# Performance work log

Hardware: AMD Instinct MI355X
Metric: run time of the kernel (lower is better)

## Reference

```python
import jax, jax.numpy as jnp
import numpy as np

EPS = 1e-8
LN_EPS = 1e-5
NEG = -1e9
H, E, D, P = 4, 32, 8, 64          # heads, embed_dim, head_dim, particles (= input_dim)
N_LAYERS, N_CLS = 4, 2
N_BATCH = 2048
F_EXTRA = 60                        # x feature channels; F_EXTRA + 4 == P == input_dim


def _ln(x):
    m = jnp.mean(x, -1, keepdims=True)
    v = jnp.mean((x - m) ** 2, -1, keepdims=True)
    return (x - m) * jax.lax.rsqrt(v + LN_EPS)


def _lin(x, w, b):
    return x @ w.T + b


def _gelu(x):
    return jax.nn.gelu(x, approximate=False)


def _mha(q_in, kv, in_w, in_b, out_w, out_b, attn_bias, kpm):
    # torch nn.MultiheadAttention, batch_first=False. q_in: (L,N,E), kv: (S,N,E)
    L, N, _ = q_in.shape
    S = kv.shape[0]
    q = _lin(q_in, in_w[:E], in_b[:E]) * (D ** -0.5)
    k = _lin(kv, in_w[E:2 * E], in_b[E:2 * E])
    v = _lin(kv, in_w[2 * E:], in_b[2 * E:])
    q = q.reshape(L, N, H, D); k = k.reshape(S, N, H, D); v = v.reshape(S, N, H, D)
    s = jnp.einsum('lnhd,snhd->nhls', q, k)
    if attn_bias is not None:
        s = s + attn_bias.reshape(N, H, L, S)
    s = jnp.where(kpm[:, None, None, :], NEG, s)
    a = jax.nn.softmax(s, -1)
    o = jnp.einsum('nhls,snhd->lnhd', a, v).reshape(L, N, E)
    return _lin(o, out_w, out_b)


def _jet_features(v):
    # vectorized calculate_jet_features_; v: (N,4,P). All pair features are symmetric,
    # diagonal stays zero (python loop skipped i==j), features are detached.
    e, px, py, pz = v[:, 0], v[:, 1], v[:, 2], v[:, 3]
    pt = jnp.sqrt(px ** 2 + py ** 2 + EPS)
    y = 0.5 * jnp.log((e + pz + EPS) / (e - pz + EPS))
    phi = jnp.mod(jnp.arctan2(py, px + EPS), 2.0 * np.pi)   # already in [0, 2pi)
    r = lambda a: a[:, :, None]
    c = lambda a: a[:, None, :]
    dist = (r(px) + c(px)) ** 2 + (r(py) + c(py)) ** 2 + (r(pz) + c(pz)) ** 2
    delta = jnp.sqrt(jnp.abs((r(y) - c(y)) ** 2 + (r(phi) - c(phi)) ** 2))
    pmin = jnp.minimum(r(pt), c(pt))
    kt = pmin * delta
    z = pmin / (r(pt) + c(pt) + EPS)
    m2 = r(e) ** 2 + c(e) ** 2 - dist
    f = jnp.stack([delta, kt, z, m2], axis=1)               # (N,4,P,P)
    f = f * (1.0 - jnp.eye(v.shape[2], dtype=f.dtype))
    return jax.lax.stop_gradient(f)


def _conv2d(x, w, b, stride, pad):
    y = jax.lax.conv_general_dilated(x, w, (stride, stride), [(pad, pad), (pad, pad)],
                                     dimension_numbers=('NCHW', 'OIHW', 'NCHW'))
    return y + b[None, :, None, None]


def _forward(x, four_momenta, jet_inputs, bn_w, bn_b, e1_w, e1_b, e2_w, e2_b,
             c1_w, c1_b, c2_w, c2_b,
             pb_in_w, pb_in_b, pb_out_w, pb_out_b, pb_f1_w, pb_f1_b, pb_f2_w, pb_f2_b, pb_wres,
             cb_in_w, cb_in_b, cb_out_w, cb_out_b, cb_f1_w, cb_f1_b, cb_f2_w, cb_f2_b, cb_wres,
             cb_cattn, cls_token, norm_w, norm_b, m1_w, m1_b, mh_w, mh_b, mf_w, mf_b):
    N = x.shape[0]
    xc = jnp.concatenate([x, four_momenta], axis=1)                 # (N, P, P): channels == particles
    kpm = ~(jnp.arange(P)[None, :] < jet_inputs[:, 1][:, None])     # (N, P) True = padded key
    xb = jnp.transpose(xc, (0, 2, 1))                               # (N, C=P, L=input_dim)
    mu = jnp.mean(xb, axis=(0, 2), keepdims=True)
    var = jnp.var(xb, axis=(0, 2), keepdims=True)
    xb = (xb - mu) * jax.lax.rsqrt(var + LN_EPS) * bn_w[None, :, None] + bn_b[None, :, None]
    h = jnp.transpose(xb, (2, 0, 1))                                # (seq, N, P)
    h = _gelu(_lin(_ln(h), e1_w, e1_b))
    h = _gelu(_lin(_ln(h), e2_w, e2_b))                             # (P, N, E)
    # --- PairEmbed: pairwise kinematic features -> 2 convs -> per-head attention bias
    f = _jet_features(four_momenta)                                 # (N, 4, P, P)
    cpe = _conv2d(f, c1_w, c1_b, 4, 0)                              # (N, H, 16, 16)
    cpe = _conv2d(cpe, c2_w, c2_b, 2, 1)                            # (N, H, 9, 9)
    bias = cpe.reshape(N * H, 9, 9)
    bias = jnp.pad(bias, ((0, 0), (0, P - 9), (0, P - 9)))          # additive bias zero-padded to (N*H,P,P)
    # --- particle blocks
    for i in range(N_LAYERS):
        res = h
        a = _ln(h)
        a = _mha(a, a, pb_in_w[i], pb_in_b[i], pb_out_w[i], pb_out_b[i], bias, kpm)
        h = _ln(a) + res
        res = h
        g = _gelu(_lin(_ln(h), pb_f1_w[i], pb_f1_b[i]))
        g = _lin(_ln(g), pb_f2_w[i], pb_f2_b[i])
        h = g + pb_wres[i] * res
    # --- class-attention blocks
    kpm_cls = jnp.concatenate([jnp.zeros((N, 1), dtype=bool), kpm], axis=1)
    cls = jnp.broadcast_to(cls_token, (1, N, E))
    for i in range(N_CLS):
        res = cls
        u = _ln(jnp.concatenate([cls, h], axis=0))                  # pre_attn_norm on keys/values only
        a = _mha(cls, u, cb_in_w[i], cb_in_b[i], cb_out_w[i], cb_out_b[i], None, kpm_cls)
        # tbhd,h->tbdh then reshape flattens as (d, h) order, matching torch
        a = jnp.einsum('tbhd,h->tbdh', a.reshape(1, N, H, D), cb_cattn[i]).reshape(1, N, E)
        cls = _ln(a) + res
        res = cls
        g = _gelu(_lin(_ln(cls), cb_f1_w[i], cb_f1_b[i]))
        g = _lin(_ln(g), cb_f2_w[i], cb_f2_b[i])
        cls = g + cb_wres[i] * res
    # --- head: affine LayerNorm + MLP (the two transposes in MLP cancel)
    z = (_ln(cls) * norm_w + norm_b)[0]                             # (N, E)
    z = jax.nn.relu(_lin(z, m1_w, m1_b))
    z = jax.nn.relu(_lin(z, mh_w, mh_b))
    z = jax.nn.sigmoid(_lin(z, mf_w, mf_b))                         # (N, 1)
    return z.reshape(-1)


def setup_inputs():
    key = jax.random.key(0)
    ks = jax.random.split(key, 40)
    w = lambda k, s: (0.05 * jax.random.normal(k, s)).astype(jnp.float32)
    p3 = jax.random.normal(ks[0], (N_BATCH, 3, P), dtype=jnp.float32)
    en = jnp.sqrt(jnp.sum(p3 ** 2, axis=1, keepdims=True) + 0.1)    # physical: E > |pz|
    four_momenta = jnp.concatenate([en, p3], axis=1)
    return {
        'x': jax.random.normal(ks[1], (N_BATCH, F_EXTRA, P), dtype=jnp.float32),
        'four_momenta': four_momenta,
        'jet_inputs': jax.random.randint(ks[2], (N_BATCH, 2), 1, P + 1),
        'bn_w': jnp.ones((P,), jnp.float32), 'bn_b': jnp.zeros((P,), jnp.float32),
        'e1_w': w(ks[3], (64, P)), 'e1_b': w(ks[4], (64,)),
        'e2_w': w(ks[5], (E, 64)), 'e2_b': w(ks[6], (E,)),
        'c1_w': w(ks[7], (H, 4, 4, 4)), 'c1_b': w(ks[8], (H,)),
        'c2_w': w(ks[9], (H, H, 2, 2)), 'c2_b': w(ks[10], (H,)),
        'pb_in_w': w(ks[11], (N_LAYERS, 3 * E, E)), 'pb_in_b': w(ks[12], (N_LAYERS, 3 * E)),
        'pb_out_w': w(ks[13], (N_LAYERS, E, E)), 'pb_out_b': w(ks[14], (N_LAYERS, E)),
        'pb_f1_w': w(ks[15], (N_LAYERS, 2 * E, E)), 'pb_f1_b': w(ks[16], (N_LAYERS, 2 * E)),
        'pb_f2_w': w(ks[17], (N_LAYERS, E, 2 * E)), 'pb_f2_b': w(ks[18], (N_LAYERS, E)),
        'pb_wres': jnp.ones((N_LAYERS, E), jnp.float32),
        'cb_in_w': w(ks[19], (N_CLS, 3 * E, E)), 'cb_in_b': w(ks[20], (N_CLS, 3 * E)),
        'cb_out_w': w(ks[21], (N_CLS, E, E)), 'cb_out_b': w(ks[22], (N_CLS, E)),
        'cb_f1_w': w(ks[23], (N_CLS, 2 * E, E)), 'cb_f1_b': w(ks[24], (N_CLS, 2 * E)),
        'cb_f2_w': w(ks[25], (N_CLS, E, 2 * E)), 'cb_f2_b': w(ks[26], (N_CLS, E)),
        'cb_wres': jnp.ones((N_CLS, E), jnp.float32),
        'cb_cattn': jnp.ones((N_CLS, H), jnp.float32),
        'cls_token': w(ks[27], (1, 1, E)),
        'norm_w': jnp.ones((E,), jnp.float32), 'norm_b': jnp.zeros((E,), jnp.float32),
        'm1_w': w(ks[28], (32, E)), 'm1_b': w(ks[29], (32,)),
        'mh_w': w(ks[30], (32, 32)), 'mh_b': w(ks[31], (32,)),
        'mf_w': w(ks[32], (1, 32)), 'mf_b': w(ks[33], (1,)),
    }


def reference(x, four_momenta, jet_inputs, bn_w, bn_b, e1_w, e1_b, e2_w, e2_b,
              c1_w, c1_b, c2_w, c2_b,
              pb_in_w, pb_in_b, pb_out_w, pb_out_b, pb_f1_w, pb_f1_b, pb_f2_w, pb_f2_b, pb_wres,
              cb_in_w, cb_in_b, cb_out_w, cb_out_b, cb_f1_w, cb_f1_b, cb_f2_w, cb_f2_b, cb_wres,
              cb_cattn, cls_token, norm_w, norm_b, m1_w, m1_b, mh_w, mh_b, mf_w, mf_b):
    return _forward(x, four_momenta, jet_inputs, bn_w, bn_b, e1_w, e1_b, e2_w, e2_b,
                    c1_w, c1_b, c2_w, c2_b,
                    pb_in_w, pb_in_b, pb_out_w, pb_out_b, pb_f1_w, pb_f1_b, pb_f2_w, pb_f2_b, pb_wres,
                    cb_in_w, cb_in_b, cb_out_w, cb_out_b, cb_f1_w, cb_f1_b, cb_f2_w, cb_f2_b, cb_wres,
                    cb_cattn, cls_token, norm_w, norm_b, m1_w, m1_b, mh_w, mh_b, mf_w, mf_b)
```

## Files before the change

kernel.cpp:

```cpp
#include <hip/hip_runtime.h>


__device__ __forceinline__ float4 ld4(const float* p){ return *reinterpret_cast<const float4*>(p); }
__device__ __forceinline__ void st4(float* p, float4 v){ *reinterpret_cast<float4*>(p) = v; }
__device__ __forceinline__ float dot4(float4 a, float4 b){ return a.x*b.x + a.y*b.y + a.z*b.z + a.w*b.w; }
__device__ __forceinline__ float geluf(float v){ return 0.5f*v*(1.0f + erff(v*0.70710678118654752f)); }

__global__ void bn_stats_partial(const float* __restrict__ x, const float* __restrict__ fm,
                                 float* __restrict__ part) {
  int p  = threadIdx.x & 63;
  int rg = threadIdx.x >> 6;
  float s = 0.f, s2 = 0.f;
  for (int R = blockIdx.x*4 + rg; R < 2048*64; R += 1024) {
    int n_ = R >> 6, c = R & 63;
    float v = (c < 60) ? x[n_*3840 + c*64 + p] : fm[n_*256 + (c-60)*64 + p];
    s += v; s2 += v*v;
  }
  __shared__ float sm[256], sm2[256];
  sm[threadIdx.x] = s; sm2[threadIdx.x] = s2;
  __syncthreads();
  if (threadIdx.x < 64) {
    part[blockIdx.x*128 + p]      = sm[p]+sm[64+p]+sm[128+p]+sm[192+p];
    part[blockIdx.x*128 + 64 + p] = sm2[p]+sm2[64+p]+sm2[128+p]+sm2[192+p];
  }
}

__global__ void bn_stats_final(const float* __restrict__ part, float* __restrict__ stats) {
  int p = threadIdx.x;
  float s = 0.f, s2 = 0.f;
  for (int b = 0; b < 256; b++){ s += part[b*128+p]; s2 += part[b*128+64+p]; }
  float mean = s * (1.f/131072.f);
  float var  = s2 * (1.f/131072.f) - mean*mean;
  stats[p]      = mean;
  stats[64+p]   = rsqrtf(var + 1e-5f);
}

__device__ __forceinline__ void ln_rows32(const float* src, float* dst, int tid){
  int r = tid>>2, g = tid&3;
  const float* row = src + r*36 + g*8;
  float4 a = ld4(row), b = ld4(row+4);
  float s = a.x+a.y+a.z+a.w + b.x+b.y+b.z+b.w;
  s += __shfl_xor(s,1); s += __shfl_xor(s,2);
  float mean = s * 0.03125f;
  float4 da = make_float4(a.x-mean,a.y-mean,a.z-mean,a.w-mean);
  float4 db = make_float4(b.x-mean,b.y-mean,b.z-mean,b.w-mean);
  float q = dot4(da,da) + dot4(db,db);
  q += __shfl_xor(q,1); q += __shfl_xor(q,2);
  float irs = rsqrtf(q*0.03125f + 1e-5f);
  float* drow = dst + r*36 + g*8;
  st4(drow,   make_float4(da.x*irs, da.y*irs, da.z*irs, da.w*irs));
  st4(drow+4, make_float4(db.x*irs, db.y*irs, db.z*irs, db.w*irs));
}

__device__ __forceinline__ void ln_rows64(const float* src, float* dst, int tid){
  int r = tid>>2, g = tid&3;
  const float* row = src + r*68 + g*16;
  float4 v0 = ld4(row), v1 = ld4(row+4), v2 = ld4(row+8), v3 = ld4(row+12);
  float s = v0.x+v0.y+v0.z+v0.w + v1.x+v1.y+v1.z+v1.w
          + v2.x+v2.y+v2.z+v2.w + v3.x+v3.y+v3.z+v3.w;
  s += __shfl_xor(s,1); s += __shfl_xor(s,2);
  float mean = s * 0.015625f;
  float4 d0 = make_float4(v0.x-mean,v0.y-mean,v0.z-mean,v0.w-mean);
  float4 d1 = make_float4(v1.x-mean,v1.y-mean,v1.z-mean,v1.w-mean);
  float4 d2 = make_float4(v2.x-mean,v2.y-mean,v2.z-mean,v2.w-mean);
  float4 d3 = make_float4(v3.x-mean,v3.y-mean,v3.z-mean,v3.w-mean);
  float q = dot4(d0,d0)+dot4(d1,d1)+dot4(d2,d2)+dot4(d3,d3);
  q += __shfl_xor(q,1); q += __shfl_xor(q,2);
  float irs = rsqrtf(q*0.015625f + 1e-5f);
  float* drow = dst + r*68 + g*16;
  st4(drow,    make_float4(d0.x*irs,d0.y*irs,d0.z*irs,d0.w*irs));
  st4(drow+4,  make_float4(d1.x*irs,d1.y*irs,d1.z*irs,d1.w*irs));
  st4(drow+8,  make_float4(d2.x*irs,d2.y*irs,d2.z*irs,d2.w*irs));
  st4(drow+12, make_float4(d3.x*irs,d3.y*irs,d3.z*irs,d3.w*irs));
}

__global__ __launch_bounds__(256, 3) void k_embed(
    const float* __restrict__ x, const float* __restrict__ fm,
    const float* __restrict__ stats,
    const float* __restrict__ bn_w, const float* __restrict__ bn_b,
    const float* __restrict__ e1w, const float* __restrict__ e1b,
    const float* __restrict__ e2w, const float* __restrict__ e2b,
    const float* __restrict__ c1w_g, const float* __restrict__ c1b_g,
    const float* __restrict__ c2w_g, const float* __restrict__ c2b_g,
    float* __restrict__ G_h, float* __restrict__ G_bias)
{
  const int n   = blockIdx.x;
  const int tid = threadIdx.x;

  __shared__ __align__(16) float SX[64*68];
  __shared__ __align__(16) float SY[64*68];
  __shared__ __align__(16) float SW[4448];
  __shared__ float SSTAT[128];

  float* PQ  = SY;
  float* C1O = SY + 448;
  float* CW  = SY + 1472;

  if (tid < 64) {
    float mu = stats[tid], rs = stats[64+tid];
    float sc = rs * bn_w[tid];
    SSTAT[tid]      = sc;
    SSTAT[64+tid]   = bn_b[tid] - mu*sc;
  }
  if (tid < 64) {
    int p = tid;
    float e_  = fm[n*256 + p];
    float px_ = fm[n*256 + 64 + p];
    float py_ = fm[n*256 + 128 + p];
    float pz_ = fm[n*256 + 192 + p];
    float pt_ = sqrtf(px_*px_ + py_*py_ + 1e-8f);
    float y_  = 0.5f * logf((e_ + pz_ + 1e-8f) / (e_ - pz_ + 1e-8f));
    float ph_ = atan2f(py_, px_ + 1e-8f);
    if (ph_ < 0.f) ph_ += 6.283185307179586f;
    PQ[0*64+p]=e_; PQ[1*64+p]=px_; PQ[2*64+p]=py_; PQ[3*64+p]=pz_;
    PQ[4*64+p]=pt_; PQ[5*64+p]=y_; PQ[6*64+p]=ph_;
  }
  CW[tid] = c1w_g[tid];
  if (tid < 4)  CW[256+tid] = c1b_g[tid];
  if (tid < 64) CW[260+tid] = c2w_g[tid];
  if (tid < 4)  CW[324+tid] = c2b_g[tid];
  __syncthreads();

  {
    int ho = tid>>4, wo = tid&15;
    float a0=0.f,a1=0.f,a2=0.f,a3=0.f;
    #pragma unroll 1
    for (int kh=0; kh<4; kh++){
      int r = ho*4+kh;
      float er=PQ[r], pxr=PQ[64+r], pyr=PQ[128+r], pzr=PQ[192+r], ptr_=PQ[256+r], yr=PQ[320+r], phr=PQ[384+r];
      #pragma unroll
      for (int kw=0; kw<4; kw++){
        int c = wo*4+kw;
        if (r == c) continue;
        float ec=PQ[c], pxc=PQ[64+c], pyc=PQ[128+c], pzc=PQ[192+c], ptc=PQ[256+c], yc=PQ[320+c], phc=PQ[384+c];
        float dy = yr-yc, dp = phr-phc;
        float delta = sqrtf(fabsf(dy*dy + dp*dp));
        float pmin = fminf(ptr_, ptc);
        float kt = pmin * delta;
        float zz = pmin / (ptr_ + ptc + 1e-8f);
        float sx_ = pxr+pxc, sy_ = pyr+pyc, sz_ = pzr+pzc;
        float m2 = er*er + ec*ec - (sx_*sx_ + sy_*sy_ + sz_*sz_);
        int wb = kh*4+kw;
        a0 += delta*CW[0*64+wb] + kt*CW[0*64+16+wb] + zz*CW[0*64+32+wb] + m2*CW[0*64+48+wb];
        a1 += delta*CW[1*64+wb] + kt*CW[1*64+16+wb] + zz*CW[1*64+32+wb] + m2*CW[1*64+48+wb];
        a2 += delta*CW[2*64+wb] + kt*CW[2*64+16+wb] + zz*CW[2*64+32+wb] + m2*CW[2*64+48+wb];
        a3 += delta*CW[3*64+wb] + kt*CW[3*64+16+wb] + zz*CW[3*64+32+wb] + m2*CW[3*64+48+wb];
      }
    }
    C1O[0*256 + tid] = a0 + CW[256+0];
    C1O[1*256 + tid] = a1 + CW[256+1];
    C1O[2*256 + tid] = a2 + CW[256+2];
    C1O[3*256 + tid] = a3 + CW[256+3];
  }
  __syncthreads();

  for (int idx = tid; idx < 324; idx += 256) {
    int co = idx/81, rem = idx%81, i = rem/9, j = rem%9;
    float s = CW[324+co];
    #pragma unroll
    for (int ci=0; ci<4; ci++){
      #pragma unroll
      for (int kh=0; kh<2; kh++){
        int ri = 2*i - 1 + kh;
        if (ri < 0 || ri >= 16) continue;
        #pragma unroll
        for (int kw=0; kw<2; kw++){
          int cj = 2*j - 1 + kw;
          if (cj < 0 || cj >= 16) continue;
          s += CW[260 + co*16 + ci*4 + kh*2 + kw] * C1O[ci*256 + ri*16 + cj];
        }
      }
    }
    G_bias[n*324 + idx] = s;
  }
  {
    int p4 = (tid & 15) * 4;
    float sc0 = SSTAT[p4], sc1 = SSTAT[p4+1], sc2 = SSTAT[p4+2], sc3 = SSTAT[p4+3];
    float sh0 = SSTAT[64+p4], sh1 = SSTAT[64+p4+1], sh2 = SSTAT[64+p4+2], sh3 = SSTAT[64+p4+3];
    for (int c = tid>>4; c < 64; c += 16) {
      float4 v = (c < 60) ? ld4(x + n*3840 + c*64 + p4) : ld4(fm + n*256 + (c-60)*64 + p4);
      st4(&SX[c*68 + p4], make_float4(v.x*sc0+sh0, v.y*sc1+sh1, v.z*sc2+sh2, v.w*sc3+sh3));
    }
  }
  __syncthreads();

  ln_rows64(SX, SY, tid);
  for (int idx = tid; idx < 1024; idx += 256) st4(&SW[(idx>>4)*68 + (idx&15)*4], ld4(e1w + idx*4));
  if (tid < 64) SW[4352+tid] = e1b[tid];
  __syncthreads();

  {
    int tg = tid>>4, og = tid&15;
    float acc[4][4];
    #pragma unroll
    for (int o=0;o<4;o++){ float b = SW[4352+o*16+og];
      #pragma unroll
      for (int i=0;i<4;i++) acc[i][o] = b; }
    #pragma unroll 2
    for (int j=0;j<64;j+=4){
      float4 av[4], wv[4];
      #pragma unroll
      for (int i=0;i<4;i++) av[i] = ld4(SY + (tg*4+i)*68 + j);
      #pragma unroll
      for (int o=0;o<4;o++) wv[o] = ld4(SW + (o*16+og)*68 + j);
      #pragma unroll
      for (int i=0;i<4;i++)
        #pragma unroll
        for (int o=0;o<4;o++) acc[i][o] += dot4(av[i], wv[o]);
    }
    __syncthreads();
    #pragma unroll
    for (int i=0;i<4;i++)
      #pragma unroll
      for (int o=0;o<4;o++) SX[(tg*4+i)*68 + o*16+og] = geluf(acc[i][o]);
  }
  __syncthreads();

  ln_rows64(SX, SY, tid);
  for (int idx = tid; idx < 512; idx += 256) st4(&SW[(idx>>4)*68 + (idx&15)*4], ld4(e2w + idx*4));
  if (tid < 32) SW[4352+tid] = e2b[tid];
  __syncthreads();

  {
    int tg = tid>>4, og = tid&15;
    float acc[4][2];
    #pragma unroll
    for (int o=0;o<2;o++){ float b = SW[4352+o*16+og];
      #pragma unroll
      for (int i=0;i<4;i++) acc[i][o] = b; }
    #pragma unroll 2
    for (int j=0;j<64;j+=4){
      float4 av[4], wv[2];
      #pragma unroll
      for (int i=0;i<4;i++) av[i] = ld4(SY + (tg*4+i)*68 + j);
      #pragma unroll
      for (int o=0;o<2;o++) wv[o] = ld4(SW + (o*16+og)*68 + j);
      #pragma unroll
      for (int i=0;i<4;i++)
        #pragma unroll
        for (int o=0;o<2;o++) acc[i][o] += dot4(av[i], wv[o]);
    }
    #pragma unroll
    for (int i=0;i<4;i++)
      #pragma unroll
      for (int o=0;o<2;o++) G_h[n*2048 + (tg*4+i)*32 + o*16+og] = geluf(acc[i][o]);
  }
}

__global__ __launch_bounds__(256, 3) void k_layer(
    const int* __restrict__ ji,
    const float* __restrict__ in_w,  const float* __restrict__ in_b,
    const float* __restrict__ out_w, const float* __restrict__ out_b,
    const float* __restrict__ f1w,   const float* __restrict__ f1b,
    const float* __restrict__ f2w,   const float* __restrict__ f2b,
    const float* __restrict__ wres,
    float* __restrict__ G_h, const float* __restrict__ G_bias)
{
  const int n   = blockIdx.x;
  const int tid = threadIdx.x;

  __shared__ __align__(16) float SH[64*36];
  __shared__ __align__(16) float SX[64*36];
  __shared__ __align__(16) float SY[64*68];
  __shared__ __align__(16) float SW[3584];
  __shared__ int s_njet;

  if (tid == 0) s_njet = ji[n*2+1];
  float b9[9];
  {
    int hh = tid>>6, l = tid&63;
    if (l < 9) {
      #pragma unroll
      for (int j=0;j<9;j++) b9[j] = G_bias[n*324 + hh*81 + l*9 + j];
    } else {
      #pragma unroll
      for (int j=0;j<9;j++) b9[j] = 0.f;
    }
  }
  for (int idx = tid; idx < 512; idx += 256) {
    float4 v = ld4(G_h + n*2048 + idx*4);
    int t = idx>>3, e = (idx&7)*4;
    st4(&SH[t*36 + e], v);
  }
  __syncthreads();

  ln_rows32(SH, SX, tid);
  for (int idx = tid; idx < 768; idx += 256) st4(&SW[(idx>>3)*36 + (idx&7)*4], ld4(in_w + idx*4));
  if (tid < 96) SW[3456+tid] = in_b[tid];
  __syncthreads();

  {
    int tg = tid>>4, og = tid&15;
    float acc[4][4];
    #pragma unroll
    for (int o=0;o<4;o++){ float b = SW[3456+32+o*16+og];
      #pragma unroll
      for (int i=0;i<4;i++) acc[i][o] = b; }
    #pragma unroll 2
    for (int j=0;j<32;j+=4){
      float4 av[4], wv[4];
      #pragma unroll
      for (int i=0;i<4;i++) av[i] = ld4(SX + (tg*4+i)*36 + j);
      #pragma unroll
      for (int o=0;o<4;o++) wv[o] = ld4(SW + (32+o*16+og)*36 + j);
      #pragma unroll
      for (int i=0;i<4;i++)
        #pragma unroll
        for (int o=0;o<4;o++) acc[i][o] += dot4(av[i], wv[o]);
    }
    #pragma unroll
    for (int i=0;i<4;i++)
      #pragma unroll
      for (int o=0;o<4;o++){
        int ew = 32 + o*16+og, t = tg*4+i;
        if (ew < 64) SY[(ew-32)*68 + t] = acc[i][o];
        else         SY[2176 + (ew-64)*68 + t] = acc[i][o];
      }
  }
  __syncthreads();

  float od[8];
  {
    int hh = tid>>6, l = tid&63;
    float qd[8];
    #pragma unroll
    for (int d=0;d<8;d++){
      int e = hh*8+d;
      float a_ = SW[3456+e];
      #pragma unroll
      for (int k=0;k<8;k++) a_ += dot4(ld4(SX + l*36 + k*4), ld4(SW + e*36 + k*4));
      qd[d] = a_ * 0.35355339059327373f;
    }
    int njet = s_njet;
    float m = -3.4e38f, lsum = 0.f;
    #pragma unroll
    for (int d=0;d<8;d++) od[d] = 0.f;
    #pragma unroll 1
    for (int s0 = 0; s0 < 64; s0 += 16) {
      if (s0 >= njet) break;
      float sc[16];
      #pragma unroll
      for (int j=0;j<16;j++) sc[j]=0.f;
      #pragma unroll
      for (int d=0;d<8;d++){
        const float* kr = SY + (hh*8+d)*68 + s0;
        float qv = qd[d];
        #pragma unroll
        for (int j=0;j<16;j+=4){
          float4 kv4 = ld4(kr+j);
          sc[j]  +=qv*kv4.x; sc[j+1]+=qv*kv4.y;
          sc[j+2]+=qv*kv4.z; sc[j+3]+=qv*kv4.w;
        }
      }
      float cm = -3.4e38f;
      if (s0 != 0 && s0 + 16 <= njet) {
        #pragma unroll
        for (int j=0;j<16;j++) cm = fmaxf(cm, sc[j]);
      } else {
        #pragma unroll
        for (int j=0;j<16;j++){
          int s = s0+j;
          float a_ = sc[j];
          if (s0 == 0 && l < 9 && j < 9) a_ += b9[j];
          a_ = (s >= njet) ? -1000000000.0f : a_;
          sc[j] = a_;
          cm = fmaxf(cm, a_);
        }
      }
      float nm = fmaxf(m, cm);
      float corr = __expf(m - nm);
      lsum *= corr;
      #pragma unroll
      for (int d=0;d<8;d++) od[d] *= corr;
      #pragma unroll
      for (int j=0;j<16;j++){ sc[j] = __expf(sc[j]-nm); lsum += sc[j]; }
      #pragma unroll
      for (int d=0;d<8;d++){
        const float* vr = SY + 2176 + (hh*8+d)*68 + s0;
        float a_ = 0.f;
        #pragma unroll
        for (int j=0;j<16;j+=4){
          float4 vv = ld4(vr+j);
          a_ += sc[j]*vv.x + sc[j+1]*vv.y + sc[j+2]*vv.z + sc[j+3]*vv.w;
        }
        od[d] += a_;
      }
      m = nm;
    }
    float inv = 1.f/lsum;
    #pragma unroll
    for (int d=0;d<8;d++) od[d] *= inv;
  }
  __syncthreads();
  {
    int hh = tid>>6, l = tid&63;
    st4(&SX[l*36 + hh*8],     make_float4(od[0],od[1],od[2],od[3]));
    st4(&SX[l*36 + hh*8 + 4], make_float4(od[4],od[5],od[6],od[7]));
  }
  for (int idx = tid; idx < 256; idx += 256) st4(&SW[(idx>>3)*36 + (idx&7)*4], ld4(out_w + idx*4));
  if (tid < 32) SW[3456+tid] = out_b[tid];
  __syncthreads();

  {
    int tg = tid>>4, og = tid&15;
    float acc[4][2];
    #pragma unroll
    for (int o=0;o<2;o++){ float b = SW[3456+o*16+og];
      #pragma unroll
      for (int i=0;i<4;i++) acc[i][o] = b; }
    #pragma unroll 2
    for (int j=0;j<32;j+=4){
      float4 av[4], wv[2];
      #pragma unroll
      for (int i=0;i<4;i++) av[i] = ld4(SX + (tg*4+i)*36 + j);
      #pragma unroll
      for (int o=0;o<2;o++) wv[o] = ld4(SW + (o*16+og)*36 + j);
      #pragma unroll
      for (int i=0;i<4;i++)
        #pragma unroll
        for (int o=0;o<2;o++) acc[i][o] += dot4(av[i], wv[o]);
    }
    #pragma unroll
    for (int i=0;i<4;i++)
      #pragma unroll
      for (int o=0;o<2;o++) SY[(tg*4+i)*36 + o*16+og] = acc[i][o];
  }
  __syncthreads();

  {
    int r = tid>>2, g = tid&3;
    const float* row = SY + r*36 + g*8;
    float4 a = ld4(row), b = ld4(row+4);
    float s = a.x+a.y+a.z+a.w + b.x+b.y+b.z+b.w;
    s += __shfl_xor(s,1); s += __shfl_xor(s,2);
    float mean = s * 0.03125f;
    float4 da = make_float4(a.x-mean,a.y-mean,a.z-mean,a.w-mean);
    float4 db = make_float4(b.x-mean,b.y-mean,b.z-mean,b.w-mean);
    float q = dot4(da,da) + dot4(db,db);
    q += __shfl_xor(q,1); q += __shfl_xor(q,2);
    float irs = rsqrtf(q*0.03125f + 1e-5f);
    float* hrow = SH + r*36 + g*8;
    float4 ha = ld4(hrow), hb = ld4(hrow+4);
    st4(hrow,   make_float4(da.x*irs+ha.x, da.y*irs+ha.y, da.z*irs+ha.z, da.w*irs+ha.w));
    st4(hrow+4, make_float4(db.x*irs+hb.x, db.y*irs+hb.y, db.z*irs+hb.z, db.w*irs+hb.w));
  }
  __syncthreads();

  ln_rows32(SH, SX, tid);
  for (int idx = tid; idx < 512; idx += 256) st4(&SW[(idx>>3)*36 + (idx&7)*4], ld4(f1w + idx*4));
  if (tid < 64) SW[3456+tid] = f1b[tid];
  __syncthreads();

  {
    int tg = tid>>4, og = tid&15;
    float acc[4][4];
    #pragma unroll
    for (int o=0;o<4;o++){ float b = SW[3456+o*16+og];
      #pragma unroll
      for (int i=0;i<4;i++) acc[i][o] = b; }
    #pragma unroll 2
    for (int j=0;j<32;j+=4){
      float4 av[4], wv[4];
      #pragma unroll
      for (int i=0;i<4;i++) av[i] = ld4(SX + (tg*4+i)*36 + j);
      #pragma unroll
      for (int o=0;o<4;o++) wv[o] = ld4(SW + (o*16+og)*36 + j);
      #pragma unroll
      for (int i=0;i<4;i++)
        #pragma unroll
        for (int o=0;o<4;o++) acc[i][o] += dot4(av[i], wv[o]);
    }
    #pragma unroll
    for (int i=0;i<4;i++)
      #pragma unroll
      for (int o=0;o<4;o++) SY[(tg*4+i)*68 + o*16+og] = geluf(acc[i][o]);
  }
  __syncthreads();

  {
    int r = tid>>2, g = tid&3;
    float* row = SY + r*68 + g*16;
    float4 v0 = ld4(row), v1 = ld4(row+4), v2 = ld4(row+8), v3 = ld4(row+12);
    float s = v0.x+v0.y+v0.z+v0.w + v1.x+v1.y+v1.z+v1.w
            + v2.x+v2.y+v2.z+v2.w + v3.x+v3.y+v3.z+v3.w;
    s += __shfl_xor(s,1); s += __shfl_xor(s,2);
    float mean = s * 0.015625f;
    float4 d0 = make_float4(v0.x-mean,v0.y-mean,v0.z-mean,v0.w-mean);
    float4 d1 = make_float4(v1.x-mean,v1.y-mean,v1.z-mean,v1.w-mean);
    float4 d2 = make_float4(v2.x-mean,v2.y-mean,v2.z-mean,v2.w-mean);
    float4 d3 = make_float4(v3.x-mean,v3.y-mean,v3.z-mean,v3.w-mean);
    float q = dot4(d0,d0)+dot4(d1,d1)+dot4(d2,d2)+dot4(d3,d3);
    q += __shfl_xor(q,1); q += __shfl_xor(q,2);
    float irs = rsqrtf(q*0.015625f + 1e-5f);
    st4(row,    make_float4(d0.x*irs,d0.y*irs,d0.z*irs,d0.w*irs));
    st4(row+4,  make_float4(d1.x*irs,d1.y*irs,d1.z*irs,d1.w*irs));
    st4(row+8,  make_float4(d2.x*irs,d2.y*irs,d2.z*irs,d2.w*irs));
    st4(row+12, make_float4(d3.x*irs,d3.y*irs,d3.z*irs,d3.w*irs));
  }
  for (int idx = tid; idx < 512; idx += 256) st4(&SW[(idx>>4)*68 + (idx&15)*4], ld4(f2w + idx*4));
  if (tid < 32){ SW[3456+tid] = f2b[tid]; SW[3488+tid] = wres[tid]; }
  __syncthreads();

  {
    int tg = tid>>4, og = tid&15;
    float acc[4][2];
    #pragma unroll
    for (int o=0;o<2;o++){ float b = SW[3456+o*16+og];
      #pragma unroll
      for (int i=0;i<4;i++) acc[i][o] = b; }
    #pragma unroll 2
    for (int j=0;j<64;j+=4){
      float4 av[4], wv[2];
      #pragma unroll
      for (int i=0;i<4;i++) av[i] = ld4(SY + (tg*4+i)*68 + j);
      #pragma unroll
      for (int o=0;o<2;o++) wv[o] = ld4(SW + (o*16+og)*68 + j);
      #pragma unroll
      for (int i=0;i<4;i++)
        #pragma unroll
        for (int o=0;o<2;o++) acc[i][o] += dot4(av[i], wv[o]);
    }
    #pragma unroll
    for (int i=0;i<4;i++)
      #pragma unroll
      for (int o=0;o<2;o++){
        int e = o*16+og, t = tg*4+i;
        G_h[n*2048 + t*32 + e] = acc[i][o] + SW[3488+e]*SH[t*36+e];
      }
  }
}

__global__ __launch_bounds__(256, 3) void k_cls(
    const int* __restrict__ ji,
    const float* __restrict__ cb_in_w, const float* __restrict__ cb_in_b,
    const float* __restrict__ cb_out_w, const float* __restrict__ cb_out_b,
    const float* __restrict__ cb_f1_w, const float* __restrict__ cb_f1_b,
    const float* __restrict__ cb_f2_w, const float* __restrict__ cb_f2_b,
    const float* __restrict__ cb_wres, const float* __restrict__ cb_cattn,
    const float* __restrict__ cls_tok, const float* __restrict__ norm_w, const float* __restrict__ norm_b,
    const float* __restrict__ m1w, const float* __restrict__ m1b,
    const float* __restrict__ mhw, const float* __restrict__ mhb,
    const float* __restrict__ mfw, const float* __restrict__ mfb,
    const float* __restrict__ G_h, float* __restrict__ out)
{
  const int n   = blockIdx.x;
  const int tid = threadIdx.x;

  __shared__ __align__(16) float SX[64*36];
  __shared__ __align__(16) float SY[64*68];
  __shared__ __align__(16) float SW[3584];
  __shared__ __align__(16) float SV[320];
  __shared__ __align__(16) float csh[32];
  __shared__ int s_njet;

  if (tid == 0) s_njet = ji[n*2+1];
  for (int idx = tid; idx < 512; idx += 256) {
    float4 v = ld4(G_h + n*2048 + idx*4);
    int t = idx>>3, e = (idx&7)*4;
    st4(&SX[t*36 + e], v);
  }
  __syncthreads();

  ln_rows32(SX, SX, tid);
  if (tid < 32) csh[tid] = cls_tok[tid];
  __syncthreads();

  #pragma unroll 1
  for (int cl = 0; cl < 2; cl++) {
    const float* iw = cb_in_w + cl*3072;
    const float* ib = cb_in_b + cl*96;

    if (tid < 32) {
      float v = csh[tid];
      float s = v;
      s += __shfl_xor(s,1); s += __shfl_xor(s,2); s += __shfl_xor(s,4); s += __shfl_xor(s,8); s += __shfl_xor(s,16);
      float mean = s * 0.03125f;
      float d = v - mean;
      float q = d*d;
      q += __shfl_xor(q,1); q += __shfl_xor(q,2); q += __shfl_xor(q,4); q += __shfl_xor(q,8); q += __shfl_xor(q,16);
      float irs = rsqrtf(q*0.03125f + 1e-5f);
      SV[tid] = d*irs;
    }
    for (int idx = tid; idx < 768; idx += 256) st4(&SW[(idx>>3)*36 + (idx&7)*4], ld4(iw + idx*4));
    if (tid < 96) SW[3456+tid] = ib[tid];
    __syncthreads();

    if (tid < 32) {
      int e = tid;
      float a_ = SW[3456+e];
      #pragma unroll
      for (int k=0;k<8;k++) a_ += dot4(ld4(&csh[k*4]), ld4(SW + e*36 + k*4));
      SV[32+e] = a_ * 0.35355339059327373f;
    }
    if (tid < 64) {
      int ew = 32 + tid;
      float a_ = SW[3456+ew];
      #pragma unroll
      for (int k=0;k<8;k++) a_ += dot4(ld4(SV + k*4), ld4(SW + ew*36 + k*4));
      if (ew < 64) SY[(ew-32)*68] = a_;
      else         SY[2176 + (ew-64)*68] = a_;
    }
    {
      int tg = tid>>4, og = tid&15;
      float acc[4][4];
      #pragma unroll
      for (int o=0;o<4;o++){ float b = SW[3456+32+o*16+og];
        #pragma unroll
        for (int i=0;i<4;i++) acc[i][o] = b; }
      #pragma unroll 2
      for (int j=0;j<32;j+=4){
        float4 av[4], wv[4];
        #pragma unroll
        for (int i=0;i<4;i++) av[i] = ld4(SX + (tg*4+i)*36 + j);
        #pragma unroll
        for (int o=0;o<4;o++) wv[o] = ld4(SW + (32+o*16+og)*36 + j);
        #pragma unroll
        for (int i=0;i<4;i++)
          #pragma unroll
          for (int o=0;o<4;o++) acc[i][o] += dot4(av[i], wv[o]);
      }
      #pragma unroll
      for (int i=0;i<4;i++)
        #pragma unroll
        for (int o=0;o<4;o++){
          int ew = 32 + o*16+og, s = tg*4+i + 1;
          if (ew < 64) SY[(ew-32)*68 + s] = acc[i][o];
          else         SY[2176 + (ew-64)*68 + s] = acc[i][o];
        }
    }
    __syncthreads();

    {
      int hh = tid>>6, l = tid&63;
      int njet = s_njet;
      float q8[8];
      #pragma unroll
      for (int d=0;d<8;d++) q8[d] = SV[32 + hh*8 + d];
      float sc_ = 0.f;
      #pragma unroll
      for (int d=0;d<8;d++) sc_ += q8[d]*SY[(hh*8+d)*68 + l];
      if (l > 0 && (l-1) >= njet) sc_ = -1000000000.0f;
      float sc64 = 0.f;
      if (l == 0){
        #pragma unroll
        for (int d=0;d<8;d++) sc64 += q8[d]*SY[(hh*8+d)*68 + 64];
        if (63 >= njet) sc64 = -1000000000.0f;
      }
      float mx = sc_;
      if (l == 0) mx = fmaxf(mx, sc64);
      mx = fmaxf(mx, __shfl_xor(mx,1));  mx = fmaxf(mx, __shfl_xor(mx,2));
      mx = fmaxf(mx, __shfl_xor(mx,4));  mx = fmaxf(mx, __shfl_xor(mx,8));
      mx = fmaxf(mx, __shfl_xor(mx,16)); mx = fmaxf(mx, __shfl_xor(mx,32));
      float p   = __expf(sc_ - mx);
      float p64 = (l==0) ? __expf(sc64 - mx) : 0.f;
      float ssum = p + p64;
      ssum += __shfl_xor(ssum,1); ssum += __shfl_xor(ssum,2); ssum += __shfl_xor(ssum,4);
      ssum += __shfl_xor(ssum,8); ssum += __shfl_xor(ssum,16); ssum += __shfl_xor(ssum,32);
      float inv = 1.f/ssum;
      #pragma unroll
      for (int d=0;d<8;d++){
        float term = p * SY[2176 + (hh*8+d)*68 + l];
        if (l == 0) term += p64 * SY[2176 + (hh*8+d)*68 + 64];
        term += __shfl_xor(term,1); term += __shfl_xor(term,2); term += __shfl_xor(term,4);
        term += __shfl_xor(term,8); term += __shfl_xor(term,16); term += __shfl_xor(term,32);
        if (l == 0) SV[64 + hh*8 + d] = term*inv;
      }
    }
    __syncthreads();

    if (tid < 32) {
      int e = tid;
      const float* wrow = cb_out_w + (cl*32 + e)*32;
      float a_ = cb_out_b[cl*32 + e];
      #pragma unroll
      for (int j=0;j<32;j++) a_ += SV[64+j]*wrow[j];
      float ca = cb_cattn[cl*4 + (e>>3)];
      SV[96 + (e&7)*4 + (e>>3)] = a_*ca;
    }
    if (tid < 32) {
      float v = SV[96+tid];
      float s = v;
      s += __shfl_xor(s,1); s += __shfl_xor(s,2); s += __shfl_xor(s,4); s += __shfl_xor(s,8); s += __shfl_xor(s,16);
      float mean = s * 0.03125f;
      float d = v - mean;
      float q = d*d;
      q += __shfl_xor(q,1); q += __shfl_xor(q,2); q += __shfl_xor(q,4); q += __shfl_xor(q,8); q += __shfl_xor(q,16);
      float irs = rsqrtf(q*0.03125f + 1e-5f);
      csh[tid] = d*irs + csh[tid];
    }
    if (tid < 32) {
      float v = csh[tid];
      float s = v;
      s += __shfl_xor(s,1); s += __shfl_xor(s,2); s += __shfl_xor(s,4); s += __shfl_xor(s,8); s += __shfl_xor(s,16);
      float mean = s * 0.03125f;
      float d = v - mean;
      float q = d*d;
      q += __shfl_xor(q,1); q += __shfl_xor(q,2); q += __shfl_xor(q,4); q += __shfl_xor(q,8); q += __shfl_xor(q,16);
      float irs = rsqrtf(q*0.03125f + 1e-5f);
      SV[tid] = d*irs;
    }
    if (tid < 64) {
      int o = tid;
      const float* wrow = cb_f1_w + (cl*64+o)*32;
      float a_ = cb_f1_b[cl*64+o];
      #pragma unroll
      for (int j=0;j<32;j++) a_ += SV[j]*wrow[j];
      SV[128+o] = geluf(a_);
    }
    if (tid < 64) {
      float v = SV[128+tid];
      float s = v;
      s += __shfl_xor(s,1); s += __shfl_xor(s,2); s += __shfl_xor(s,4); s += __shfl_xor(s,8);
      s += __shfl_xor(s,16); s += __shfl_xor(s,32);
      float mean = s * 0.015625f;
      float d = v - mean;
      float q = d*d;
      q += __shfl_xor(q,1); q += __shfl_xor(q,2); q += __shfl_xor(q,4); q += __shfl_xor(q,8);
      q += __shfl_xor(q,16); q += __shfl_xor(q,32);
      float irs = rsqrtf(q*0.015625f + 1e-5f);
      SV[192+tid] = d*irs;
    }
    if (tid < 32) {
      int e = tid;
      const float* wrow = cb_f2_w + (cl*32+e)*64;
      float a_ = cb_f2_b[cl*32+e];
      #pragma unroll
      for (int j=0;j<64;j++) a_ += SV[192+j]*wrow[j];
      csh[e] = a_ + cb_wres[cl*32+e]*csh[e];
    }
  }

  if (tid < 32) {
    float v = csh[tid];
    float s = v;
    s += __shfl_xor(s,1); s += __shfl_xor(s,2); s += __shfl_xor(s,4); s += __shfl_xor(s,8); s += __shfl_xor(s,16);
    float mean = s * 0.03125f;
    float d = v - mean;
    float q = d*d;
    q += __shfl_xor(q,1); q += __shfl_xor(q,2); q += __shfl_xor(q,4); q += __shfl_xor(q,8); q += __shfl_xor(q,16);
    float irs = rsqrtf(q*0.03125f + 1e-5f);
    SV[tid] = d*irs*norm_w[tid] + norm_b[tid];
  }
  if (tid < 32) {
    float a_ = m1b[tid];
    const float* wrow = m1w + tid*32;
    #pragma unroll
    for (int j=0;j<32;j++) a_ += SV[j]*wrow[j];
    SV[64+tid] = fmaxf(a_, 0.f);
  }
  if (tid < 32) {
    float a_ = mhb[tid];
    const float* wrow = mhw + tid*32;
    #pragma unroll
    for (int j=0;j<32;j++) a_ += SV[64+j]*wrow[j];
    SV[128+tid] = fmaxf(a_, 0.f);
  }
  if (tid == 0) {
    float a_ = mfb[0];
    #pragma unroll
    for (int j=0;j<32;j++) a_ += SV[128+j]*mfw[j];
    out[n] = 1.f/(1.f + expf(-a_));
  }
}

extern "C" void kernel_launch(void* const* d_in, const int* in_sizes, int n_in,
                              void* d_out, int out_size, void* d_ws, size_t ws_size,
                              hipStream_t stream) {
  (void)in_sizes; (void)n_in; (void)out_size; (void)ws_size;
  const float* x     = (const float*)d_in[0];
  const float* fm    = (const float*)d_in[1];
  const int*   ji    = (const int*)  d_in[2];
  const float* bn_w  = (const float*)d_in[3];
  const float* bn_b  = (const float*)d_in[4];
  const float* e1w   = (const float*)d_in[5];
  const float* e1b   = (const float*)d_in[6];
  const float* e2w   = (const float*)d_in[7];
  const float* e2b   = (const float*)d_in[8];
  const float* c1w   = (const float*)d_in[9];
  const float* c1b   = (const float*)d_in[10];
  const float* c2w   = (const float*)d_in[11];
  const float* c2b   = (const float*)d_in[12];
  const float* pb_in_w  = (const float*)d_in[13];
  const float* pb_in_b  = (const float*)d_in[14];
  const float* pb_out_w = (const float*)d_in[15];
  const float* pb_out_b = (const float*)d_in[16];
  const float* pb_f1_w  = (const float*)d_in[17];
  const float* pb_f1_b  = (const float*)d_in[18];
  const float* pb_f2_w  = (const float*)d_in[19];
  const float* pb_f2_b  = (const float*)d_in[20];
  const float* pb_wres  = (const float*)d_in[21];
  const float* cb_in_w  = (const float*)d_in[22];
  const float* cb_in_b  = (const float*)d_in[23];
  const float* cb_out_w = (const float*)d_in[24];
  const float* cb_out_b = (const float*)d_in[25];
  const float* cb_f1_w  = (const float*)d_in[26];
  const float* cb_f1_b  = (const float*)d_in[27];
  const float* cb_f2_w  = (const float*)d_in[28];
  const float* cb_f2_b  = (const float*)d_in[29];
  const float* cb_wres  = (const float*)d_in[30];
  const float* cb_cattn = (const float*)d_in[31];
  const float* cls_tok  = (const float*)d_in[32];
  const float* norm_w   = (const float*)d_in[33];
  const float* norm_b   = (const float*)d_in[34];
  const float* m1w      = (const float*)d_in[35];
  const float* m1b      = (const float*)d_in[36];
  const float* mhw      = (const float*)d_in[37];
  const float* mhb      = (const float*)d_in[38];
  const float* mfw      = (const float*)d_in[39];
  const float* mfb      = (const float*)d_in[40];

  float* part   = (float*)d_ws;
  float* stats  = part + 32768;
  float* G_h    = part + 40960;
  float* G_bias = G_h + 2048*2048;

  bn_stats_partial<<<256, 256, 0, stream>>>(x, fm, part);
  bn_stats_final<<<1, 64, 0, stream>>>(part, stats);
  k_embed<<<2048, 256, 0, stream>>>(x, fm, stats, bn_w, bn_b, e1w, e1b, e2w, e2b,
                                    c1w, c1b, c2w, c2b, G_h, G_bias);
  for (int li = 0; li < 4; li++) {
    k_layer<<<2048, 256, 0, stream>>>(ji,
        pb_in_w + li*3072, pb_in_b + li*96,
        pb_out_w + li*1024, pb_out_b + li*32,
        pb_f1_w + li*2048, pb_f1_b + li*64,
        pb_f2_w + li*2048, pb_f2_b + li*32,
        pb_wres + li*32, G_h, G_bias);
  }
  k_cls<<<2048, 256, 0, stream>>>(ji, cb_in_w, cb_in_b, cb_out_w, cb_out_b,
                                  cb_f1_w, cb_f1_b, cb_f2_w, cb_f2_b,
                                  cb_wres, cb_cattn, cls_tok, norm_w, norm_b,
                                  m1w, m1b, mhw, mhb, mfw, mfb, G_h, (float*)d_out);
}
```

Baseline: 512.5 us.

## Skip per-token work for padded particles beyond each jet's count

Each kernel reads the per-jet particle count and gates the layernorm, projection, MLP and output stages on whether a wave's 16-token slice contains any real particles. It also loads only the hidden rows up to the rounded particle count and zero-fills keys for inactive slices in the class-attention kernel. Whole wavefronts of work on masked padding tokens are skipped. This relies on padded tokens never affecting outputs, and padded rows of the hidden state become stale or uninitialised.

```diff
diff --git a/kernel.cpp b/kernel.cpp
--- a/kernel.cpp
+++ b/kernel.cpp
@@ -76,6 +76,7 @@
 
 __global__ __launch_bounds__(256, 3) void k_embed(
     const float* __restrict__ x, const float* __restrict__ fm,
+    const int* __restrict__ ji,
     const float* __restrict__ stats,
     const float* __restrict__ bn_w, const float* __restrict__ bn_b,
     const float* __restrict__ e1w, const float* __restrict__ e1b,
@@ -86,6 +87,8 @@
 {
   const int n   = blockIdx.x;
   const int tid = threadIdx.x;
+  const int njet = ji[n*2+1];
+  const bool wact = ((tid>>6)<<4) < njet;
 
   __shared__ __align__(16) float SX[64*68];
   __shared__ __align__(16) float SY[64*68];
@@ -184,7 +187,7 @@
   }
   __syncthreads();
 
-  ln_rows64(SX, SY, tid);
+  if (wact) ln_rows64(SX, SY, tid);
   for (int idx = tid; idx < 1024; idx += 256) st4(&SW[(idx>>4)*68 + (idx&15)*4], ld4(e1w + idx*4));
   if (tid < 64) SW[4352+tid] = e1b[tid];
   __syncthreads();
@@ -196,32 +199,36 @@
     for (int o=0;o<4;o++){ float b = SW[4352+o*16+og];
       #pragma unroll
       for (int i=0;i<4;i++) acc[i][o] = b; }
-    #pragma unroll 2
-    for (int j=0;j<64;j+=4){
-      float4 av[4], wv[4];
-      #pragma unroll
-      for (int i=0;i<4;i++) av[i] = ld4(SY + (tg*4+i)*68 + j);
-      #pragma unroll
-      for (int o=0;o<4;o++) wv[o] = ld4(SW + (o*16+og)*68 + j);
+    if (wact) {
+      #pragma unroll 2
+      for (int j=0;j<64;j+=4){
+        float4 av[4], wv[4];
+        #pragma unroll
+        for (int i=0;i<4;i++) av[i] = ld4(SY + (tg*4+i)*68 + j);
+        #pragma unroll
+        for (int o=0;o<4;o++) wv[o] = ld4(SW + (o*16+og)*68 + j);
+        #pragma unroll
+        for (int i=0;i<4;i++)
+          #pragma unroll
+          for (int o=0;o<4;o++) acc[i][o] += dot4(av[i], wv[o]);
+      }
+    }
+    __syncthreads();
+    if (wact) {
       #pragma unroll
       for (int i=0;i<4;i++)
         #pragma unroll
-        for (int o=0;o<4;o++) acc[i][o] += dot4(av[i], wv[o]);
-    }
-    __syncthreads();
-    #pragma unroll
-    for (int i=0;i<4;i++)
-      #pragma unroll
-      for (int o=0;o<4;o++) SX[(tg*4+i)*68 + o*16+og] = geluf(acc[i][o]);
-  }
-  __syncthreads();
-
-  ln_rows64(SX, SY, tid);
+        for (int o=0;o<4;o++) SX[(tg*4+i)*68 + o*16+og] = geluf(acc[i][o]);
+    }
+  }
+  __syncthreads();
+
+  if (wact) ln_rows64(SX, SY, tid);
   for (int idx = tid; idx < 512; idx += 256) st4(&SW[(idx>>4)*68 + (idx&15)*4], ld4(e2w + idx*4));
   if (tid < 32) SW[4352+tid] = e2b[tid];
   __syncthreads();
 
-  {
+  if (wact) {
     int tg = tid>>4, og = tid&15;
     float acc[4][2];
     #pragma unroll
@@ -258,14 +265,15 @@
 {
   const int n   = blockIdx.x;
   const int tid = threadIdx.x;
+  const int njet = ji[n*2+1];
+  const int nt16 = (njet + 15) & ~15;
+  const bool wact = ((tid>>6)<<4) < njet;
 
   __shared__ __align__(16) float SH[64*36];
   __shared__ __align__(16) float SX[64*36];
   __shared__ __align__(16) float SY[64*68];
   __shared__ __align__(16) float SW[3584];
-  __shared__ int s_njet;
-
-  if (tid == 0) s_njet = ji[n*2+1];
+
   float b9[9];
   {
     int hh = tid>>6, l = tid&63;
@@ -277,19 +285,19 @@
       for (int j=0;j<9;j++) b9[j] = 0.f;
     }
   }
-  for (int idx = tid; idx < 512; idx += 256) {
+  for (int idx = tid; idx < (nt16<<3); idx += 256) {
     float4 v = ld4(G_h + n*2048 + idx*4);
     int t = idx>>3, e = (idx&7)*4;
     st4(&SH[t*36 + e], v);
   }
   __syncthreads();
 
-  ln_rows32(SH, SX, tid);
+  if (wact) ln_rows32(SH, SX, tid);
   for (int idx = tid; idx < 768; idx += 256) st4(&SW[(idx>>3)*36 + (idx&7)*4], ld4(in_w + idx*4));
   if (tid < 96) SW[3456+tid] = in_b[tid];
   __syncthreads();
 
-  {
+  if (wact) {
     int tg = tid>>4, og = tid&15;
     float acc[4][4];
     #pragma unroll
@@ -331,13 +339,11 @@
       for (int k=0;k<8;k++) a_ += dot4(ld4(SX + l*36 + k*4), ld4(SW + e*36 + k*4));
       qd[d] = a_ * 0.35355339059327373f;
     }
-    int njet = s_njet;
     float m = -3.4e38f, lsum = 0.f;
     #pragma unroll
     for (int d=0;d<8;d++) od[d] = 0.f;
     #pragma unroll 1
-    for (int s0 = 0; s0 < 64; s0 += 16) {
-      if (s0 >= njet) break;
+    for (int s0 = 0; s0 < njet; s0 += 16) {
       float sc[16];
       #pragma unroll
       for (int j=0;j<16;j++) sc[j]=0.f;
@@ -401,7 +407,7 @@
   if (tid < 32) SW[3456+tid] = out_b[tid];
   __syncthreads();
 
-  {
+  if (wact) {
     int tg = tid>>4, og = tid&15;
     float acc[4][2];
     #pragma unroll
@@ -427,7 +433,7 @@
   }
   __syncthreads();
 
-  {
+  if (wact) {
     int r = tid>>2, g = tid&3;
     const float* row = SY + r*36 + g*8;
     float4 a = ld4(row), b = ld4(row+4);
@@ -446,12 +452,12 @@
   }
   __syncthreads();
 
-  ln_rows32(SH, SX, tid);
+  if (wact) ln_rows32(SH, SX, tid);
   for (int idx = tid; idx < 512; idx += 256) st4(&SW[(idx>>3)*36 + (idx&7)*4], ld4(f1w + idx*4));
   if (tid < 64) SW[3456+tid] = f1b[tid];
   __syncthreads();
 
-  {
+  if (wact) {
     int tg = tid>>4, og = tid&15;
     float acc[4][4];
     #pragma unroll
@@ -477,7 +483,7 @@
   }
   __syncthreads();
 
-  {
+  if (wact) {
     int r = tid>>2, g = tid&3;
     float* row = SY + r*68 + g*16;
     float4 v0 = ld4(row), v1 = ld4(row+4), v2 = ld4(row+8), v3 = ld4(row+12);
@@ -501,7 +507,7 @@
   if (tid < 32){ SW[3456+tid] = f2b[tid]; SW[3488+tid] = wres[tid]; }
   __syncthreads();
 
-  {
+  if (wact) {
     int tg = tid>>4, og = tid&15;
     float acc[4][2];
     #pragma unroll
@@ -545,23 +551,24 @@
 {
   const int n   = blockIdx.x;
   const int tid = threadIdx.x;
+  const int njet = ji[n*2+1];
+  const int nt16 = (njet + 15) & ~15;
+  const bool wact = ((tid>>6)<<4) < njet;
 
   __shared__ __align__(16) float SX[64*36];
   __shared__ __align__(16) float SY[64*68];
   __shared__ __align__(16) float SW[3584];
   __shared__ __align__(16) float SV[320];
   __shared__ __align__(16) float csh[32];
-  __shared__ int s_njet;
-
-  if (tid == 0) s_njet = ji[n*2+1];
-  for (int idx = tid; idx < 512; idx += 256) {
+
+  for (int idx = tid; idx < (nt16<<3); idx += 256) {
     float4 v = ld4(G_h + n*2048 + idx*4);
     int t = idx>>3, e = (idx&7)*4;
     st4(&SX[t*36 + e], v);
   }
   __syncthreads();
 
-  ln_rows32(SX, SX, tid);
+  if (wact) ln_rows32(SX, SX, tid);
   if (tid < 32) csh[tid] = cls_tok[tid];
   __syncthreads();
 
@@ -602,37 +609,47 @@
     }
     {
       int tg = tid>>4, og = tid&15;
-      float acc[4][4];
-      #pragma unroll
-      for (int o=0;o<4;o++){ float b = SW[3456+32+o*16+og];
-        #pragma unroll
-        for (int i=0;i<4;i++) acc[i][o] = b; }
-      #pragma unroll 2
-      for (int j=0;j<32;j+=4){
-        float4 av[4], wv[4];
-        #pragma unroll
-        for (int i=0;i<4;i++) av[i] = ld4(SX + (tg*4+i)*36 + j);
-        #pragma unroll
-        for (int o=0;o<4;o++) wv[o] = ld4(SW + (32+o*16+og)*36 + j);
+      if (wact) {
+        float acc[4][4];
+        #pragma unroll
+        for (int o=0;o<4;o++){ float b = SW[3456+32+o*16+og];
+          #pragma unroll
+          for (int i=0;i<4;i++) acc[i][o] = b; }
+        #pragma unroll 2
+        for (int j=0;j<32;j+=4){
+          float4 av[4], wv[4];
+          #pragma unroll
+          for (int i=0;i<4;i++) av[i] = ld4(SX + (tg*4+i)*36 + j);
+          #pragma unroll
+          for (int o=0;o<4;o++) wv[o] = ld4(SW + (32+o*16+og)*36 + j);
+          #pragma unroll
+          for (int i=0;i<4;i++)
+            #pragma unroll
+            for (int o=0;o<4;o++) acc[i][o] += dot4(av[i], wv[o]);
+        }
         #pragma unroll
         for (int i=0;i<4;i++)
           #pragma unroll
-          for (int o=0;o<4;o++) acc[i][o] += dot4(av[i], wv[o]);
-      }
-      #pragma unroll
-      for (int i=0;i<4;i++)
-        #pragma unroll
-        for (int o=0;o<4;o++){
-          int ew = 32 + o*16+og, s = tg*4+i + 1;
-          if (ew < 64) SY[(ew-32)*68 + s] = acc[i][o];
-          else         SY[2176 + (ew-64)*68 + s] = acc[i][o];
-        }
+          for (int o=0;o<4;o++){
+            int ew = 32 + o*16+og, s = tg*4+i + 1;
+            if (ew < 64) SY[(ew-32)*68 + s] = acc[i][o];
+            else         SY[2176 + (ew-64)*68 + s] = acc[i][o];
+          }
+      } else {
+        #pragma unroll
+        for (int i=0;i<4;i++)
+          #pragma unroll
+          for (int o=0;o<4;o++){
+            int ew = 32 + o*16+og, s = tg*4+i + 1;
+            if (ew < 64) SY[(ew-32)*68 + s] = 0.f;
+            else         SY[2176 + (ew-64)*68 + s] = 0.f;
+          }
+      }
     }
     __syncthreads();
 
     {
       int hh = tid>>6, l = tid&63;
-      int njet = s_njet;
       float q8[8];
       #pragma unroll
       for (int d=0;d<8;d++) q8[d] = SV[32 + hh*8 + d];
@@ -816,7 +833,7 @@
 
   bn_stats_partial<<<256, 256, 0, stream>>>(x, fm, part);
   bn_stats_final<<<1, 64, 0, stream>>>(part, stats);
-  k_embed<<<2048, 256, 0, stream>>>(x, fm, stats, bn_w, bn_b, e1w, e1b, e2w, e2b,
+  k_embed<<<2048, 256, 0, stream>>>(x, fm, ji, stats, bn_w, bn_b, e1w, e1b, e2w, e2b,
                                     c1w, c1b, c2w, c2b, G_h, G_bias);
   for (int li = 0; li < 4; li++) {
     k_layer<<<2048, 256, 0, stream>>>(ji,
```

After: 498.5 us. 1.03x faster.
